# Optimization experiments

Hardware: AMD Instinct MI355X
Metric: run time of the kernel (lower is better)

## Reference

```python
import jax, jax.numpy as jnp
import numpy as np


def gru_cell(x, h, wi, wh, bi, bh):
    # torch.nn.GRUCell math
    gi = x @ wi.T + bi  # (B, 3*H)
    gh = h @ wh.T + bh
    i_r, i_z, i_n = jnp.split(gi, 3, axis=-1)
    h_r, h_z, h_n = jnp.split(gh, 3, axis=-1)
    r = jax.nn.sigmoid(i_r + h_r)
    z = jax.nn.sigmoid(i_z + h_z)
    n = jnp.tanh(i_n + r * h_n)
    return (1.0 - z) * n + z * h


def setup_inputs() -> dict:
    key = jax.random.key(0)
    B, T = 256, 512
    dim_ctx, dim_mel, r = 512, 160, 2
    dim_pre, dim_att = 128, 256
    dim_rnn = dim_att + dim_ctx  # 768
    ks = jax.random.split(key, 32)
    rn = lambda k, shp, s=0.05: jax.random.normal(k, shp, jnp.float32) * s
    w = jax.random.uniform(ks[1], (B, T), jnp.float32)
    w = w / jnp.sum(w, axis=1, keepdims=True)  # valid attention distribution
    return {
        "x": rn(ks[0], (B, r, dim_mel // r), 1.0),
        "w": w,
        "h_att": jnp.zeros((B, dim_att), jnp.float32),
        "h_dec0": jnp.zeros((B, dim_rnn), jnp.float32),
        "h_dec1": jnp.zeros((B, dim_rnn), jnp.float32),
        "memory": rn(ks[2], (B, T, dim_ctx), 1.0),
        # PreNet: Linear(dim_mel->dim_pre)+ReLU, Linear(dim_pre->dim_pre)+ReLU
        "pre_w1": rn(ks[3], (dim_pre, dim_mel)), "pre_b1": rn(ks[4], (dim_pre,)),
        "pre_w2": rn(ks[5], (dim_pre, dim_pre)), "pre_b2": rn(ks[6], (dim_pre,)),
        # attention GRUCell (dim_pre -> dim_att)
        "att_wi": rn(ks[7], (3 * dim_att, dim_pre)), "att_wh": rn(ks[8], (3 * dim_att, dim_att)),
        "att_bi": rn(ks[9], (3 * dim_att,)), "att_bh": rn(ks[10], (3 * dim_att,)),
        # ContentMarkovAttention query projection (dim_att -> dim_ctx)
        "q_w": rn(ks[11], (dim_ctx, dim_att)), "q_b": rn(ks[12], (dim_ctx,)),
        # ResGRUCell 0 (dim_rnn -> dim_rnn)
        "dec0_wi": rn(ks[13], (3 * dim_rnn, dim_rnn)), "dec0_wh": rn(ks[14], (3 * dim_rnn, dim_rnn)),
        "dec0_bi": rn(ks[15], (3 * dim_rnn,)), "dec0_bh": rn(ks[16], (3 * dim_rnn,)),
        # ResGRUCell 1
        "dec1_wi": rn(ks[17], (3 * dim_rnn, dim_rnn)), "dec1_wh": rn(ks[18], (3 * dim_rnn, dim_rnn)),
        "dec1_bi": rn(ks[19], (3 * dim_rnn,)), "dec1_bh": rn(ks[20], (3 * dim_rnn,)),
    }


def reference(x, w, h_att, h_dec0, h_dec1, memory,
              pre_w1, pre_b1, pre_w2, pre_b2,
              att_wi, att_wh, att_bi, att_bh,
              q_w, q_b,
              dec0_wi, dec0_wh, dec0_bi, dec0_bh,
              dec1_wi, dec1_wh, dec1_bi, dec1_bh):
    B = x.shape[0]
    # PreNet on flattened r*mel frames
    xf = x.reshape(B, -1)
    h = jax.nn.relu(xf @ pre_w1.T + pre_b1)
    h = jax.nn.relu(h @ pre_w2.T + pre_b2)  # (B, dim_pre)
    # context vector with PREVIOUS attention weights (matches bmm before update)
    ctx = jnp.einsum('bt,btc->bc', w, memory)
    # attention GRU
    h_att_new = gru_cell(h, h_att, att_wi, att_wh, att_bi, att_bh)
    # ContentMarkovAttention: content scores * Markov (stay/move) prior, renormalized
    q = h_att_new @ q_w.T + q_b  # (B, dim_ctx)
    e = jnp.einsum('btc,bc->bt', memory, q) / jnp.sqrt(jnp.float32(memory.shape[-1]))
    a = jax.nn.softmax(e, axis=-1)
    w_shift = jnp.concatenate([jnp.zeros_like(w[:, :1]), w[:, :-1]], axis=1)
    w_prior = 0.5 * (w + w_shift)
    w_new = a * w_prior
    w_new = w_new / (jnp.sum(w_new, axis=1, keepdims=True) + 1e-8)
    # stacked residual GRU cells on [h_att; ctx]
    x_dec = jnp.concatenate([h_att_new, ctx], axis=1)  # (B, dim_rnn)
    h0 = gru_cell(x_dec, h_dec0, dec0_wi, dec0_wh, dec0_bi, dec0_bh) + x_dec
    h1 = gru_cell(h0, h_dec1, dec1_wi, dec1_wh, dec1_bi, dec1_bh) + h0
    return h1, w_new, h_att_new, h0, h1
```

## Files before the change

### kernel.cpp

```cpp
#include <hip/hip_runtime.h>
#include <math.h>

#define B    256
#define T    512
#define CTX  512
#define MEL  160
#define PRE  128
#define ATT  256
#define RNN  768
#define G3   2304

typedef __attribute__((ext_vector_type(8))) short short8;
typedef __attribute__((ext_vector_type(4))) float f32x4;

__device__ __forceinline__ unsigned short f2bf(float f) {
    unsigned u = __float_as_uint(f);
    unsigned r = (u + 0x7fffu + ((u >> 16) & 1u)) >> 16;
    return (unsigned short)r;
}
__device__ __forceinline__ float bf2f(unsigned short h) {
    return __uint_as_float((unsigned)h << 16);
}

__device__ __forceinline__ void conv8(const float* p, short8* hi8, short8* lo8) {
    const float4 v0 = *(const float4*)p;
    const float4 v1 = *(const float4*)(p + 4);
    const float av[8] = {v0.x, v0.y, v0.z, v0.w, v1.x, v1.y, v1.z, v1.w};
    short hi[8], lo[8];
    #pragma unroll
    for (int u = 0; u < 8; ++u) {
        const unsigned short h = f2bf(av[u]);
        hi[u] = (short)h;
        lo[u] = (short)f2bf(av[u] - bf2f(h));
    }
    *hi8 = *(const short8*)hi;
    *lo8 = *(const short8*)lo;
}

__device__ __forceinline__ void gemm64_body(
        const float* __restrict__ A, const float* __restrict__ W,
        float* __restrict__ C, int m0, int n0, int tid,
        short* AH, short* AL, short* WH, short* WL) {
    const int lane = tid & 63;
    const int wave = tid >> 6;
    const int wm = wave >> 1, wn = wave & 1;

    f32x4 acc[2][2] = {{{0.f, 0.f, 0.f, 0.f}, {0.f, 0.f, 0.f, 0.f}},
                       {{0.f, 0.f, 0.f, 0.f}, {0.f, 0.f, 0.f, 0.f}}};

    for (int k0 = 0; k0 < RNN; k0 += 64) {
        #pragma unroll
        for (int si = 0; si < 2; ++si) {
            const int s = tid + si * 256;
            const int sub = s >> 6;
            const int ln = s & 63;
            const int row = (sub >> 1) * 16 + (ln & 15);
            const int kk = (sub & 1) * 32 + (ln >> 4) * 8;
            conv8(A + (size_t)(m0 + row) * RNN + k0 + kk,
                  (short8*)&AH[s * 8], (short8*)&AL[s * 8]);
            conv8(W + (size_t)(n0 + row) * RNN + k0 + kk,
                  (short8*)&WH[s * 8], (short8*)&WL[s * 8]);
        }
        __syncthreads();

        #pragma unroll
        for (int ks = 0; ks < 2; ++ks) {
            short8 ah[2], al[2], wh[2], wl[2];
            #pragma unroll
            for (int i = 0; i < 2; ++i) {
                const int asub = ((wm * 2 + i) * 2 + ks);
                ah[i] = *(const short8*)&AH[(asub * 64 + lane) * 8];
                al[i] = *(const short8*)&AL[(asub * 64 + lane) * 8];
                const int wsub = ((wn * 2 + i) * 2 + ks);
                wh[i] = *(const short8*)&WH[(wsub * 64 + lane) * 8];
                wl[i] = *(const short8*)&WL[(wsub * 64 + lane) * 8];
            }
            #pragma unroll
            for (int i = 0; i < 2; ++i)
                #pragma unroll
                for (int j = 0; j < 2; ++j) {
                    acc[i][j] = __builtin_amdgcn_mfma_f32_16x16x32_bf16(ah[i], wh[j], acc[i][j], 0, 0, 0);
                    acc[i][j] = __builtin_amdgcn_mfma_f32_16x16x32_bf16(al[i], wh[j], acc[i][j], 0, 0, 0);
                    acc[i][j] = __builtin_amdgcn_mfma_f32_16x16x32_bf16(ah[i], wl[j], acc[i][j], 0, 0, 0);
                }
        }
        __syncthreads();
    }

    const int rowq = lane >> 4, col = lane & 15;
    #pragma unroll
    for (int i = 0; i < 2; ++i)
        #pragma unroll
        for (int j = 0; j < 2; ++j) {
            const int rbase = m0 + wm * 32 + i * 16 + rowq * 4;
            const int cidx = n0 + wn * 32 + j * 16 + col;
            #pragma unroll
            for (int r = 0; r < 4; ++r)
                C[(size_t)(rbase + r) * G3 + cidx] = acc[i][j][r];
        }
}

__global__ __launch_bounds__(256) void prep_kernel(
        const float* __restrict__ pw1, const float* __restrict__ pw2,
        const float* __restrict__ wi, const float* __restrict__ wh,
        const float* __restrict__ qw,
        short* __restrict__ p1h, short* __restrict__ p1l,
        short* __restrict__ p2h, short* __restrict__ p2l,
        short* __restrict__ wih, short* __restrict__ wil,
        short* __restrict__ whh, short* __restrict__ whl,
        short* __restrict__ qwh, short* __restrict__ qwl,
        const float* __restrict__ h_dec0, const float* __restrict__ dec0_wh,
        const float* __restrict__ h_dec1, const float* __restrict__ dec1_wh,
        float* __restrict__ gh0, float* __restrict__ gh1) {
    __shared__ __align__(16) short AH[4096];
    __shared__ __align__(16) short AL[4096];
    __shared__ __align__(16) short WH[4096];
    __shared__ __align__(16) short WL[4096];
    const int blk = blockIdx.x;
    const int tid = threadIdx.x;

    if (blk < 226) {
        int s = blk * 256 + tid;
        const float* src; short *dh, *dl; int K, KS, slot;
        if (s < 2560)                  { src = pw1; dh = p1h; dl = p1l; K = MEL; KS = 5; slot = s; }
        else if ((s -= 2560) < 2048)   { src = pw2; dh = p2h; dl = p2l; K = PRE; KS = 4; slot = s; }
        else if ((s -= 2048) < 12288)  { src = wi;  dh = wih; dl = wil; K = PRE; KS = 4; slot = s; }
        else if ((s -= 12288) < 24576) { src = wh;  dh = whh; dl = whl; K = ATT; KS = 8; slot = s; }
        else if ((s -= 24576) < 16384) { src = qw;  dh = qwh; dl = qwl; K = ATT; KS = 8; slot = s; }
        else return;
        const int lane = slot & 63;
        const int ks = (slot >> 6) % KS;
        const int nt = (slot >> 6) / KS;
        const int n = nt * 16 + (lane & 15);
        const int k = ks * 32 + (lane >> 4) * 8;
        conv8(src + (size_t)n * K + k,
              (short8*)(dh + (size_t)slot * 8), (short8*)(dl + (size_t)slot * 8));
        return;
    }
    const int u = blk - 226;
    const float* A; const float* W; float* C;
    int r;
    if (u < 144) { A = h_dec0; W = dec0_wh; C = gh0; r = u; }
    else         { A = h_dec1; W = dec1_wh; C = gh1; r = u - 144; }
    gemm64_body(A, W, C, (r / 36) * 64, (r % 36) * 64, tid, AH, AL, WH, WL);
}

__global__ __launch_bounds__(512) void front_mfma_kernel(
        const float* __restrict__ x, const float* __restrict__ b1,
        const float* __restrict__ b2, const float* __restrict__ h_att,
        const float* __restrict__ bi, const float* __restrict__ bh,
        const float* __restrict__ qb,
        const short* __restrict__ p1h, const short* __restrict__ p1l,
        const short* __restrict__ p2h, const short* __restrict__ p2l,
        const short* __restrict__ wih, const short* __restrict__ wil,
        const short* __restrict__ whh, const short* __restrict__ whl,
        const short* __restrict__ qwh, const short* __restrict__ qwl,
        float* __restrict__ h_att_out, float* __restrict__ x_dec,
        float* __restrict__ q) {
    __shared__ __align__(16) short AH[8][64][8];
    __shared__ __align__(16) short AL[8][64][8];
    __shared__ __align__(16) float S[16][RNN];
    __shared__ __align__(16) float S2[16][RNN];
    __shared__ __align__(16) float hs[16][ATT];

    const int tid = threadIdx.x;
    const int wave = tid >> 6, lane = tid & 63;
    const int mb = blockIdx.x * 16;
    const int col = lane & 15, rowq = lane >> 4;

    for (int i = tid; i < 16 * ATT; i += 512)
        hs[i >> 8][i & 255] = h_att[(size_t)(mb + (i >> 8)) * ATT + (i & 255)];
    if (tid < 320) {
        const int sub = tid >> 6, ln = tid & 63;
        const int row = ln & 15, kk = sub * 32 + (ln >> 4) * 8;
        conv8(x + (size_t)(mb + row) * MEL + kk, (short8*)AH[sub][ln], (short8*)AL[sub][ln]);
    }
    __syncthreads();

    {
        const int nt = wave;
        f32x4 acc = {0.f, 0.f, 0.f, 0.f};
        #pragma unroll
        for (int ks = 0; ks < 5; ++ks) {
            const short8 a_h = *(const short8*)AH[ks][lane];
            const short8 a_l = *(const short8*)AL[ks][lane];
            const size_t fo = ((size_t)(nt * 5 + ks) * 64 + lane) * 8;
            const short8 b_h = *(const short8*)(p1h + fo);
            const short8 b_l = *(const short8*)(p1l + fo);
            acc = __builtin_amdgcn_mfma_f32_16x16x32_bf16(a_h, b_h, acc, 0, 0, 0);
            acc = __builtin_amdgcn_mfma_f32_16x16x32_bf16(a_l, b_h, acc, 0, 0, 0);
            acc = __builtin_amdgcn_mfma_f32_16x16x32_bf16(a_h, b_l, acc, 0, 0, 0);
        }
        const int j = nt * 16 + col;
        const float bb = b1[j];
        #pragma unroll
        for (int r = 0; r < 4; ++r)
            S[rowq * 4 + r][j] = fmaxf(acc[r] + bb, 0.f);
    }
    __syncthreads();
    if (tid < 256) {
        const int sub = tid >> 6, ln = tid & 63;
        const int row = ln & 15, kk = sub * 32 + (ln >> 4) * 8;
        conv8(&S[row][kk], (short8*)AH[sub][ln], (short8*)AL[sub][ln]);
    }
    __syncthreads();

    {
        const int nt = wave;
        f32x4 acc = {0.f, 0.f, 0.f, 0.f};
        #pragma unroll
        for (int ks = 0; ks < 4; ++ks) {
            const short8 a_h = *(const short8*)AH[ks][lane];
            const short8 a_l = *(const short8*)AL[ks][lane];
            const size_t fo = ((size_t)(nt * 4 + ks) * 64 + lane) * 8;
            const short8 b_h = *(const short8*)(p2h + fo);
            const short8 b_l = *(const short8*)(p2l + fo);
            acc = __builtin_amdgcn_mfma_f32_16x16x32_bf16(a_h, b_h, acc, 0, 0, 0);
            acc = __builtin_amdgcn_mfma_f32_16x16x32_bf16(a_l, b_h, acc, 0, 0, 0);
            acc = __builtin_amdgcn_mfma_f32_16x16x32_bf16(a_h, b_l, acc, 0, 0, 0);
        }
        const int j = wave * 16 + col;
        const float bb = b2[j];
        #pragma unroll
        for (int r = 0; r < 4; ++r)
            S[rowq * 4 + r][j] = fmaxf(acc[r] + bb, 0.f);
    }
    __syncthreads();
    if (tid < 256) {
        const int sub = tid >> 6, ln = tid & 63;
        const int row = ln & 15, kk = sub * 32 + (ln >> 4) * 8;
        conv8(&S[row][kk], (short8*)AH[sub][ln], (short8*)AL[sub][ln]);
    }
    __syncthreads();

    for (int t = 0; t < 6; ++t) {
        const int nt = wave * 6 + t;
        f32x4 acc = {0.f, 0.f, 0.f, 0.f};
        #pragma unroll
        for (int ks = 0; ks < 4; ++ks) {
            const short8 a_h = *(const short8*)AH[ks][lane];
            const short8 a_l = *(const short8*)AL[ks][lane];
            const size_t fo = ((size_t)(nt * 4 + ks) * 64 + lane) * 8;
            const short8 b_h = *(const short8*)(wih + fo);
            const short8 b_l = *(const short8*)(wil + fo);
            acc = __builtin_amdgcn_mfma_f32_16x16x32_bf16(a_h, b_h, acc, 0, 0, 0);
            acc = __builtin_amdgcn_mfma_f32_16x16x32_bf16(a_l, b_h, acc, 0, 0, 0);
            acc = __builtin_amdgcn_mfma_f32_16x16x32_bf16(a_h, b_l, acc, 0, 0, 0);
        }
        const int j = nt * 16 + col;
        #pragma unroll
        for (int r = 0; r < 4; ++r) S[rowq * 4 + r][j] = acc[r];
    }
    __syncthreads();
    {
        const int sub = tid >> 6, ln = tid & 63;
        const int row = ln & 15, kk = sub * 32 + (ln >> 4) * 8;
        conv8(&hs[row][kk], (short8*)AH[sub][ln], (short8*)AL[sub][ln]);
    }
    __syncthreads();

    for (int t = 0; t < 6; ++t) {
        const int nt = wave * 6 + t;
        f32x4 acc = {0.f, 0.f, 0.f, 0.f};
        #pragma unroll
        for (int ks = 0; ks < 8; ++ks) {
            const short8 a_h = *(const short8*)AH[ks][lane];
            const short8 a_l = *(const short8*)AL[ks][lane];
            const size_t fo = ((size_t)(nt * 8 + ks) * 64 + lane) * 8;
            const short8 b_h = *(const short8*)(whh + fo);
            const short8 b_l = *(const short8*)(whl + fo);
            acc = __builtin_amdgcn_mfma_f32_16x16x32_bf16(a_h, b_h, acc, 0, 0, 0);
            acc = __builtin_amdgcn_mfma_f32_16x16x32_bf16(a_l, b_h, acc, 0, 0, 0);
            acc = __builtin_amdgcn_mfma_f32_16x16x32_bf16(a_h, b_l, acc, 0, 0, 0);
        }
        const int j = nt * 16 + col;
        #pragma unroll
        for (int r = 0; r < 4; ++r) S2[rowq * 4 + r][j] = acc[r];
    }
    __syncthreads();

    for (int e = tid; e < 16 * ATT; e += 512) {
        const int b = e >> 8, j = e & 255;
        const float ir = S[b][j] + bi[j];
        const float iz = S[b][ATT + j] + bi[ATT + j];
        const float in_ = S[b][2 * ATT + j] + bi[2 * ATT + j];
        const float hr = S2[b][j] + bh[j];
        const float hz = S2[b][ATT + j] + bh[ATT + j];
        const float hn = S2[b][2 * ATT + j] + bh[2 * ATT + j];
        const float r = 1.f / (1.f + expf(-(ir + hr)));
        const float z = 1.f / (1.f + expf(-(iz + hz)));
        const float n = tanhf(in_ + r * hn);
        const float hnew = (1.f - z) * n + z * hs[b][j];
        h_att_out[(size_t)(mb + b) * ATT + j] = hnew;
        x_dec[(size_t)(mb + b) * RNN + j] = hnew;
        hs[b][j] = hnew;
    }
    __syncthreads();
    {
        const int sub = tid >> 6, ln = tid & 63;
        const int row = ln & 15, kk = sub * 32 + (ln >> 4) * 8;
        conv8(&hs[row][kk], (short8*)AH[sub][ln], (short8*)AL[sub][ln]);
    }
    __syncthreads();

    for (int t = 0; t < 4; ++t) {
        const int nt = wave * 4 + t;
        f32x4 acc = {0.f, 0.f, 0.f, 0.f};
        #pragma unroll
        for (int ks = 0; ks < 8; ++ks) {
            const short8 a_h = *(const short8*)AH[ks][lane];
            const short8 a_l = *(const short8*)AL[ks][lane];
            const size_t fo = ((size_t)(nt * 8 + ks) * 64 + lane) * 8;
            const short8 b_h = *(const short8*)(qwh + fo);
            const short8 b_l = *(const short8*)(qwl + fo);
            acc = __builtin_amdgcn_mfma_f32_16x16x32_bf16(a_h, b_h, acc, 0, 0, 0);
            acc = __builtin_amdgcn_mfma_f32_16x16x32_bf16(a_l, b_h, acc, 0, 0, 0);
            acc = __builtin_amdgcn_mfma_f32_16x16x32_bf16(a_h, b_l, acc, 0, 0, 0);
        }
        const int j = nt * 16 + col;
        const float bb = qb[j];
        #pragma unroll
        for (int r = 0; r < 4; ++r)
            q[(size_t)(mb + rowq * 4 + r) * CTX + j] = acc[r] + bb;
    }
}

__global__ __launch_bounds__(512) void attn_kernel(
        const float* __restrict__ mem, const float* __restrict__ w,
        const float* __restrict__ q, float* __restrict__ x_dec,
        float* __restrict__ w_new) {
    __shared__ float qs[CTX];
    __shared__ float ws_[T];
    __shared__ float e_s[T];
    __shared__ float ctx_s[8][CTX];
    __shared__ float red[8];

    const int b = blockIdx.x;
    const int tid = threadIdx.x;
    const int wave = tid >> 6, lane = tid & 63;

    if (tid < CTX) qs[tid] = q[(size_t)b * CTX + tid];
    ws_[tid] = w[(size_t)b * T + tid];
    __syncthreads();

    const int c0 = lane * 4;
    const int c1 = 256 + lane * 4;
    const float q0 = qs[c0], q1 = qs[c0 + 1], q2 = qs[c0 + 2], q3 = qs[c0 + 3];
    const float q4 = qs[c1], q5 = qs[c1 + 1], q6 = qs[c1 + 2], q7 = qs[c1 + 3];

    const float* mb = mem + (size_t)b * T * CTX;
    float acc[8] = {0.f, 0.f, 0.f, 0.f, 0.f, 0.f, 0.f, 0.f};
    const float invs = 0.04419417382415922f;
    const int t0 = wave * 64;

    #pragma unroll 4
    for (int i = 0; i < 64; ++i) {
        const int t = t0 + i;
        const float* row = mb + (size_t)t * CTX;
        const float4 m0 = *(const float4*)(row + c0);
        const float4 m1 = *(const float4*)(row + c1);
        const float wt = ws_[t];
        float ep = m0.x * q0 + m0.y * q1 + m0.z * q2 + m0.w * q3
                 + m1.x * q4 + m1.y * q5 + m1.z * q6 + m1.w * q7;
        #pragma unroll
        for (int off = 32; off; off >>= 1) ep += __shfl_xor(ep, off);
        if (lane == 0) e_s[t] = ep * invs;
        acc[0] += wt * m0.x; acc[1] += wt * m0.y; acc[2] += wt * m0.z; acc[3] += wt * m0.w;
        acc[4] += wt * m1.x; acc[5] += wt * m1.y; acc[6] += wt * m1.z; acc[7] += wt * m1.w;
    }
    ctx_s[wave][c0] = acc[0]; ctx_s[wave][c0 + 1] = acc[1]; ctx_s[wave][c0 + 2] = acc[2]; ctx_s[wave][c0 + 3] = acc[3];
    ctx_s[wave][c1] = acc[4]; ctx_s[wave][c1 + 1] = acc[5]; ctx_s[wave][c1 + 2] = acc[6]; ctx_s[wave][c1 + 3] = acc[7];
    __syncthreads();

    {
        const int c = tid;
        float s = 0.f;
        #pragma unroll
        for (int wv = 0; wv < 8; ++wv) s += ctx_s[wv][c];
        x_dec[(size_t)b * RNN + ATT + c] = s;
    }

    const float ev = e_s[tid];
    float m = ev;
    #pragma unroll
    for (int o = 32; o; o >>= 1) m = fmaxf(m, __shfl_xor(m, o));
    if (lane == 0) red[wave] = m;
    __syncthreads();
    m = red[0];
    #pragma unroll
    for (int wv = 1; wv < 8; ++wv) m = fmaxf(m, red[wv]);
    __syncthreads();

    const float x0 = expf(ev - m);
    float s = x0;
    #pragma unroll
    for (int o = 32; o; o >>= 1) s += __shfl_xor(s, o);
    if (lane == 0) red[wave] = s;
    __syncthreads();
    s = red[0] + red[1] + red[2] + red[3] + red[4] + red[5] + red[6] + red[7];
    __syncthreads();

    const float p = 0.5f * (ws_[tid] + (tid > 0 ? ws_[tid - 1] : 0.f));
    const float m0v = (x0 / s) * p;
    float s2 = m0v;
    #pragma unroll
    for (int o = 32; o; o >>= 1) s2 += __shfl_xor(s2, o);
    if (lane == 0) red[wave] = s2;
    __syncthreads();
    s2 = red[0] + red[1] + red[2] + red[3] + red[4] + red[5] + red[6] + red[7];
    w_new[(size_t)b * T + tid] = m0v / (s2 + 1e-8f);
}

__global__ __launch_bounds__(256) void gemm_gi_kernel(
        const float* __restrict__ A, const float* __restrict__ W,
        float* __restrict__ C) {
    __shared__ __align__(16) short AH[4096];
    __shared__ __align__(16) short AL[4096];
    __shared__ __align__(16) short WH[4096];
    __shared__ __align__(16) short WL[4096];
    gemm64_body(A, W, C, blockIdx.y * 64, blockIdx.x * 64, threadIdx.x, AH, AL, WH, WL);
}

__global__ void gru_res_kernel(const float* __restrict__ gi, const float* __restrict__ gh,
                               const float* __restrict__ x_in, const float* __restrict__ h_prev,
                               const float* __restrict__ bi, const float* __restrict__ bh,
                               float* __restrict__ out0, float* __restrict__ out1) {
    const int idx = blockIdx.x * 256 + threadIdx.x;
    const int b = idx / RNN, j = idx % RNN;
    const float* gib = gi + (size_t)b * G3;
    const float* ghb = gh + (size_t)b * G3;
    const float ir = gib[j] + bi[j];
    const float iz = gib[RNN + j] + bi[RNN + j];
    const float in_ = gib[2 * RNN + j] + bi[2 * RNN + j];
    const float hr = ghb[j] + bh[j];
    const float hz = ghb[RNN + j] + bh[RNN + j];
    const float hn = ghb[2 * RNN + j] + bh[2 * RNN + j];
    const float r = 1.f / (1.f + expf(-(ir + hr)));
    const float z = 1.f / (1.f + expf(-(iz + hz)));
    const float n = tanhf(in_ + r * hn);
    const float res = (1.f - z) * n + z * h_prev[idx] + x_in[idx];
    out0[idx] = res;
    if (out1) out1[idx] = res;
}

extern "C" void kernel_launch(void* const* d_in, const int* in_sizes, int n_in,
                              void* d_out, int out_size, void* d_ws, size_t ws_size,
                              hipStream_t stream) {
    const float* x       = (const float*)d_in[0];
    const float* w       = (const float*)d_in[1];
    const float* h_att   = (const float*)d_in[2];
    const float* h_dec0  = (const float*)d_in[3];
    const float* h_dec1  = (const float*)d_in[4];
    const float* memory  = (const float*)d_in[5];
    const float* pre_w1  = (const float*)d_in[6];
    const float* pre_b1  = (const float*)d_in[7];
    const float* pre_w2  = (const float*)d_in[8];
    const float* pre_b2  = (const float*)d_in[9];
    const float* att_wi  = (const float*)d_in[10];
    const float* att_wh  = (const float*)d_in[11];
    const float* att_bi  = (const float*)d_in[12];
    const float* att_bh  = (const float*)d_in[13];
    const float* q_w     = (const float*)d_in[14];
    const float* q_b     = (const float*)d_in[15];
    const float* dec0_wi = (const float*)d_in[16];
    const float* dec0_wh = (const float*)d_in[17];
    const float* dec0_bi = (const float*)d_in[18];
    const float* dec0_bh = (const float*)d_in[19];
    const float* dec1_wi = (const float*)d_in[20];
    const float* dec1_wh = (const float*)d_in[21];
    const float* dec1_bi = (const float*)d_in[22];
    const float* dec1_bh = (const float*)d_in[23];

    float* out = (float*)d_out;
    float* o_h1a = out;
    float* o_wn  = out + 196608;
    float* o_ha  = out + 327680;
    float* o_h0  = out + 393216;
    float* o_h1b = out + 589824;

    float* ws    = (float*)d_ws;
    float* q     = ws;
    float* x_dec = ws + 131072;
    float* gi    = ws + 327680;
    float* gh0   = ws + 917504;
    float* gh1   = ws + 1507328;
    short* sb    = (short*)(ws + 2097152);
    short* p1h = sb;             short* p1l = sb + 20480;
    short* p2h = sb + 40960;     short* p2l = sb + 57344;
    short* wih = sb + 73728;     short* wil = sb + 172032;
    short* whh = sb + 270336;    short* whl = sb + 466944;
    short* qwh = sb + 663552;    short* qwl = sb + 794624;

    prep_kernel<<<514, 256, 0, stream>>>(pre_w1, pre_w2, att_wi, att_wh, q_w,
                                         p1h, p1l, p2h, p2l, wih, wil, whh, whl, qwh, qwl,
                                         h_dec0, dec0_wh, h_dec1, dec1_wh, gh0, gh1);
    front_mfma_kernel<<<16, 512, 0, stream>>>(x, pre_b1, pre_b2, h_att, att_bi, att_bh, q_b,
                                              p1h, p1l, p2h, p2l, wih, wil, whh, whl, qwh, qwl,
                                              o_ha, x_dec, q);
    attn_kernel<<<B, 512, 0, stream>>>(memory, w, q, x_dec, o_wn);

    gemm_gi_kernel<<<dim3(36, 4), 256, 0, stream>>>(x_dec, dec0_wi, gi);
    gru_res_kernel<<<768, 256, 0, stream>>>(gi, gh0, x_dec, h_dec0, dec0_bi, dec0_bh, o_h0, nullptr);

    gemm_gi_kernel<<<dim3(36, 4), 256, 0, stream>>>(o_h0, dec1_wi, gi);
    gru_res_kernel<<<768, 256, 0, stream>>>(gi, gh1, o_h0, h_dec1, dec1_bi, dec1_bh, o_h1a, o_h1b);
}
```

Baseline: 192.2 us.

## Split attention memory pass across T-slices with last-block atomic finalize

```diff
diff --git a/kernel.cpp b/kernel.cpp
--- a/kernel.cpp
+++ b/kernel.cpp
@@ -111,7 +111,8 @@
         short* __restrict__ qwh, short* __restrict__ qwl,
         const float* __restrict__ h_dec0, const float* __restrict__ dec0_wh,
         const float* __restrict__ h_dec1, const float* __restrict__ dec1_wh,
-        float* __restrict__ gh0, float* __restrict__ gh1) {
+        float* __restrict__ gh0, float* __restrict__ gh1,
+        unsigned* __restrict__ rowcnt) {
     __shared__ __align__(16) short AH[4096];
     __shared__ __align__(16) short AL[4096];
     __shared__ __align__(16) short WH[4096];
@@ -120,6 +121,7 @@
     const int tid = threadIdx.x;
 
     if (blk < 226) {
+        if (blk == 0) rowcnt[tid] = 0;
         int s = blk * 256 + tid;
         const float* src; short *dh, *dl; int K, KS, slot;
         if (s < 2560)                  { src = pw1; dh = p1h; dl = p1l; K = MEL; KS = 5; slot = s; }
@@ -325,22 +327,18 @@
     }
 }
 
-__global__ __launch_bounds__(512) void attn_kernel(
-        const float* __restrict__ mem, const float* __restrict__ w,
-        const float* __restrict__ q, float* __restrict__ x_dec,
-        float* __restrict__ w_new) {
-    __shared__ float qs[CTX];
-    __shared__ float ws_[T];
-    __shared__ float e_s[T];
-    __shared__ float ctx_s[8][CTX];
-    __shared__ float red[8];
-
-    const int b = blockIdx.x;
+__global__ void mempass_mid_kernel(const float* __restrict__ mem, const float* __restrict__ w,
+                                   const float* __restrict__ q, float* __restrict__ e,
+                                   float* __restrict__ ctx_part, float* __restrict__ x_dec,
+                                   float* __restrict__ w_new, unsigned* __restrict__ rowcnt) {
+    const int b = blockIdx.y, slice = blockIdx.x;
     const int tid = threadIdx.x;
     const int wave = tid >> 6, lane = tid & 63;
-
-    if (tid < CTX) qs[tid] = q[(size_t)b * CTX + tid];
-    ws_[tid] = w[(size_t)b * T + tid];
+    __shared__ float qs[CTX];
+    __shared__ float ctx_s[4][CTX];
+    __shared__ float red[4];
+    __shared__ int last_s;
+    for (int i = tid; i < CTX; i += 256) qs[i] = q[(size_t)b * CTX + i];
     __syncthreads();
 
     const int c0 = lane * 4;
@@ -351,64 +349,83 @@
     const float* mb = mem + (size_t)b * T * CTX;
     float acc[8] = {0.f, 0.f, 0.f, 0.f, 0.f, 0.f, 0.f, 0.f};
     const float invs = 0.04419417382415922f;
-    const int t0 = wave * 64;
+    const int t0 = slice * 64 + wave * 16;
 
     #pragma unroll 4
-    for (int i = 0; i < 64; ++i) {
+    for (int i = 0; i < 16; ++i) {
         const int t = t0 + i;
         const float* row = mb + (size_t)t * CTX;
         const float4 m0 = *(const float4*)(row + c0);
         const float4 m1 = *(const float4*)(row + c1);
-        const float wt = ws_[t];
+        const float wt = w[(size_t)b * T + t];
         float ep = m0.x * q0 + m0.y * q1 + m0.z * q2 + m0.w * q3
                  + m1.x * q4 + m1.y * q5 + m1.z * q6 + m1.w * q7;
         #pragma unroll
         for (int off = 32; off; off >>= 1) ep += __shfl_xor(ep, off);
-        if (lane == 0) e_s[t] = ep * invs;
+        if (lane == 0) e[(size_t)b * T + t] = ep * invs;
         acc[0] += wt * m0.x; acc[1] += wt * m0.y; acc[2] += wt * m0.z; acc[3] += wt * m0.w;
         acc[4] += wt * m1.x; acc[5] += wt * m1.y; acc[6] += wt * m1.z; acc[7] += wt * m1.w;
     }
     ctx_s[wave][c0] = acc[0]; ctx_s[wave][c0 + 1] = acc[1]; ctx_s[wave][c0 + 2] = acc[2]; ctx_s[wave][c0 + 3] = acc[3];
     ctx_s[wave][c1] = acc[4]; ctx_s[wave][c1 + 1] = acc[5]; ctx_s[wave][c1 + 2] = acc[6]; ctx_s[wave][c1 + 3] = acc[7];
     __syncthreads();
-
-    {
-        const int c = tid;
+    for (int c = tid; c < CTX; c += 256) {
+        const float s = ctx_s[0][c] + ctx_s[1][c] + ctx_s[2][c] + ctx_s[3][c];
+        ctx_part[((size_t)slice * B + b) * CTX + c] = s;
+    }
+
+    __threadfence();
+    __syncthreads();
+    if (tid == 0) {
+        const unsigned prev = __hip_atomic_fetch_add(&rowcnt[b], 1u,
+                                  __ATOMIC_ACQ_REL, __HIP_MEMORY_SCOPE_AGENT);
+        last_s = (prev == 7u) ? 1 : 0;
+    }
+    __syncthreads();
+    if (!last_s) return;
+    __threadfence();
+
+    for (int c = tid; c < CTX; c += 256) {
         float s = 0.f;
         #pragma unroll
-        for (int wv = 0; wv < 8; ++wv) s += ctx_s[wv][c];
+        for (int sl = 0; sl < 8; ++sl) s += ctx_part[((size_t)sl * B + b) * CTX + c];
         x_dec[(size_t)b * RNN + ATT + c] = s;
     }
 
-    const float ev = e_s[tid];
-    float m = ev;
+    const float* eb = e + (size_t)b * T;
+    const float* wb = w + (size_t)b * T;
+    const float e0 = eb[tid], e1 = eb[tid + 256];
+
+    float m = fmaxf(e0, e1);
     #pragma unroll
     for (int o = 32; o; o >>= 1) m = fmaxf(m, __shfl_xor(m, o));
     if (lane == 0) red[wave] = m;
     __syncthreads();
-    m = red[0];
-    #pragma unroll
-    for (int wv = 1; wv < 8; ++wv) m = fmaxf(m, red[wv]);
-    __syncthreads();
-
-    const float x0 = expf(ev - m);
-    float s = x0;
+    m = fmaxf(fmaxf(red[0], red[1]), fmaxf(red[2], red[3]));
+    __syncthreads();
+
+    const float x0 = expf(e0 - m), x1 = expf(e1 - m);
+    float s = x0 + x1;
     #pragma unroll
     for (int o = 32; o; o >>= 1) s += __shfl_xor(s, o);
     if (lane == 0) red[wave] = s;
     __syncthreads();
-    s = red[0] + red[1] + red[2] + red[3] + red[4] + red[5] + red[6] + red[7];
-    __syncthreads();
-
-    const float p = 0.5f * (ws_[tid] + (tid > 0 ? ws_[tid - 1] : 0.f));
-    const float m0v = (x0 / s) * p;
-    float s2 = m0v;
+    s = red[0] + red[1] + red[2] + red[3];
+    __syncthreads();
+
+    const float p0 = 0.5f * (wb[tid] + (tid > 0 ? wb[tid - 1] : 0.f));
+    const float p1 = 0.5f * (wb[tid + 256] + wb[tid + 255]);
+    const float m0 = (x0 / s) * p0;
+    const float m1 = (x1 / s) * p1;
+    float s2 = m0 + m1;
     #pragma unroll
     for (int o = 32; o; o >>= 1) s2 += __shfl_xor(s2, o);
     if (lane == 0) red[wave] = s2;
     __syncthreads();
-    s2 = red[0] + red[1] + red[2] + red[3] + red[4] + red[5] + red[6] + red[7];
-    w_new[(size_t)b * T + tid] = m0v / (s2 + 1e-8f);
+    s2 = red[0] + red[1] + red[2] + red[3];
+    const float inv = 1.f / (s2 + 1e-8f);
+    w_new[(size_t)b * T + tid] = m0 * inv;
+    w_new[(size_t)b * T + tid + 256] = m1 * inv;
 }
 
 __global__ __launch_bounds__(256) void gemm_gi_kernel(
@@ -478,13 +495,16 @@
     float* o_h0  = out + 393216;
     float* o_h1b = out + 589824;
 
-    float* ws    = (float*)d_ws;
-    float* q     = ws;
-    float* x_dec = ws + 131072;
-    float* gi    = ws + 327680;
-    float* gh0   = ws + 917504;
-    float* gh1   = ws + 1507328;
-    short* sb    = (short*)(ws + 2097152);
+    float* ws     = (float*)d_ws;
+    float* q      = ws;
+    float* x_dec  = ws + 131072;
+    float* gi     = ws + 327680;
+    float* gh0    = ws + 917504;
+    float* gh1    = ws + 1507328;
+    float* ctxp   = ws + 2097152;
+    float* e      = ws + 3145728;
+    unsigned* rowcnt = (unsigned*)(ws + 3276800);
+    short* sb     = (short*)(ws + 3277056);
     short* p1h = sb;             short* p1l = sb + 20480;
     short* p2h = sb + 40960;     short* p2l = sb + 57344;
     short* wih = sb + 73728;     short* wil = sb + 172032;
@@ -493,11 +513,11 @@
 
     prep_kernel<<<514, 256, 0, stream>>>(pre_w1, pre_w2, att_wi, att_wh, q_w,
                                          p1h, p1l, p2h, p2l, wih, wil, whh, whl, qwh, qwl,
-                                         h_dec0, dec0_wh, h_dec1, dec1_wh, gh0, gh1);
+                                         h_dec0, dec0_wh, h_dec1, dec1_wh, gh0, gh1, rowcnt);
     front_mfma_kernel<<<16, 512, 0, stream>>>(x, pre_b1, pre_b2, h_att, att_bi, att_bh, q_b,
                                               p1h, p1l, p2h, p2l, wih, wil, whh, whl, qwh, qwl,
                                               o_ha, x_dec, q);
-    attn_kernel<<<B, 512, 0, stream>>>(memory, w, q, x_dec, o_wn);
+    mempass_mid_kernel<<<dim3(8, B), 256, 0, stream>>>(memory, w, q, e, ctxp, x_dec, o_wn, rowcnt);
 
     gemm_gi_kernel<<<dim3(36, 4), 256, 0, stream>>>(x_dec, dec0_wi, gi);
     gru_res_kernel<<<768, 256, 0, stream>>>(gi, gh0, x_dec, h_dec0, dec0_bi, dec0_bh, o_h0, nullptr);
```

Measured after the change: 595.3 us. 3.1x slower.
